# Optimization experiments

Hardware: AMD Instinct MI355X
Metric: run time of the kernel (lower is better)

The kernel has to match this reference:

```python
import jax, jax.numpy as jnp
import numpy as np

N_EMBD = 1024
N_HEAD = 16
HEAD_DIM = N_EMBD // N_HEAD


def setup_inputs() -> dict:
    key = jax.random.key(0)
    ks = jax.random.split(key, 6)
    B, T, C = 4, 2048, N_EMBD
    scale = 1.0 / np.sqrt(C)
    x = jax.random.normal(ks[0], (B, T, C), dtype=jnp.float32)
    Wq = jax.random.normal(ks[1], (C, C), dtype=jnp.float32) * scale
    Wk = jax.random.normal(ks[2], (C, C), dtype=jnp.float32) * scale
    Wv = jax.random.normal(ks[3], (C, C), dtype=jnp.float32) * scale
    Wo = jax.random.normal(ks[4], (C, C), dtype=jnp.float32) * scale
    bo = jax.random.normal(ks[5], (C,), dtype=jnp.float32) * 0.01
    return {"x": x, "Wq": Wq, "Wk": Wk, "Wv": Wv, "Wo": Wo, "bo": bo}


def reference(x, Wq, Wk, Wv, Wo, bo):
    B, T, C = x.shape
    H, D = N_HEAD, HEAD_DIM
    # projections (torch Linear: x @ W.T); reshape to [B, H, T, D]
    q = (x @ Wq.T).reshape(B, T, H, D).transpose(0, 2, 1, 3)
    k = (x @ Wk.T).reshape(B, T, H, D).transpose(0, 2, 1, 3)
    v = (x @ Wv.T).reshape(B, T, H, D).transpose(0, 2, 1, 3)
    scores = jnp.einsum("bhqd,bhkd->bhqk", q, k) / np.sqrt(D)
    causal = jnp.tril(jnp.ones((T, T), dtype=bool))  # True = keep
    scores = jnp.where(causal, scores, -jnp.inf)
    attn = jax.nn.softmax(scores, axis=-1)
    # dropout in eval mode = identity
    out = jnp.einsum("bhqk,bhkd->bhqd", attn, v)
    out = out.transpose(0, 2, 1, 3).reshape(B, T, C)
    return out @ Wo.T + bo
```

## Files before the change

### kernel.cpp

```cpp
#include <hip/hip_runtime.h>

typedef __attribute__((ext_vector_type(4))) float floatx4;
typedef __attribute__((ext_vector_type(8))) __bf16 bf16x8;
typedef __attribute__((ext_vector_type(8))) unsigned short ushort8;
typedef __attribute__((ext_vector_type(4))) unsigned short ushort4v;

#define MFMA16(a, b, c) __builtin_amdgcn_mfma_f32_16x16x32_bf16((a), (b), (c), 0, 0, 0)

static __device__ __forceinline__ unsigned short f2bu(float f) {
  unsigned int u = __builtin_bit_cast(unsigned int, f);
  unsigned int r = (u + 0x7fffu + ((u >> 16) & 1u)) >> 16;
  return (unsigned short)r;
}

static __device__ __forceinline__ unsigned int cvtpk(float lo, float hi) {
  unsigned int r;
  asm("v_cvt_pk_bf16_f32 %0, %1, %2" : "=v"(r) : "v"(lo), "v"(hi));
  return r;
}

static __device__ __forceinline__ float fexp2(float x) {
  float r;
  asm("v_exp_f32 %0, %1" : "=v"(r) : "v"(x));
  return r;
}

static __device__ __forceinline__ void gload_lds16(const void* g, void* l) {
  __builtin_amdgcn_global_load_lds((const __attribute__((address_space(1))) void*)g,
                                   (__attribute__((address_space(3))) void*)l, 16, 0, 0);
}

__global__ void cast_f32_bf16(const float* __restrict__ src, unsigned short* __restrict__ dst, int n4) {
  int i = blockIdx.x * blockDim.x + threadIdx.x;
  if (i >= n4) return;
  float4 v = reinterpret_cast<const float4*>(src)[i];
  ushort4v o;
  o.x = f2bu(v.x); o.y = f2bu(v.y); o.z = f2bu(v.z); o.w = f2bu(v.w);
  reinterpret_cast<ushort4v*>(dst)[i] = o;
}

static __device__ __forceinline__ void gemm_core(const unsigned short* __restrict__ Ag,
                                                 const unsigned short* __restrict__ Wg,
                                                 int tm0, int tn0,
                                                 unsigned short* As, unsigned short* Bs,
                                                 floatx4 acc[4][4]) {
  const int tid = threadIdx.x;
  const int w = tid >> 6, l = tid & 63;
  const int lg = l >> 4, lq = l & 15;
  const int wr = w >> 1, wc = w & 1;

  const int srow = w * 32 + (l >> 2);
  const int scol = (l & 3) * 8;
  const unsigned short* ga = Ag + (size_t)(tm0 + srow) * 1024 + scol;
  const unsigned short* gb = Wg + (size_t)(tn0 + srow) * 1024 + scol;
  unsigned short* la0 = As + (w * 32) * 32;
  unsigned short* la1 = la0 + 16 * 32;
  unsigned short* lb0 = Bs + (w * 32) * 32;
  unsigned short* lb1 = lb0 + 16 * 32;

  for (int kt = 0; kt < 32; ++kt) {
    gload_lds16(ga + kt * 32, la0);
    gload_lds16(ga + 16 * 1024 + kt * 32, la1);
    gload_lds16(gb + kt * 32, lb0);
    gload_lds16(gb + 16 * 1024 + kt * 32, lb1);
    __syncthreads();
    bf16x8 ar[4], br[4];
#pragma unroll
    for (int i = 0; i < 4; ++i) {
      ar[i] = *(const bf16x8*)(As + (wr * 64 + i * 16 + lq) * 32 + lg * 8);
      br[i] = *(const bf16x8*)(Bs + (wc * 64 + i * 16 + lq) * 32 + lg * 8);
    }
#pragma unroll
    for (int i = 0; i < 4; ++i)
#pragma unroll
      for (int j = 0; j < 4; ++j)
        acc[i][j] = MFMA16(ar[i], br[j], acc[i][j]);
    __syncthreads();
  }
}

__global__ __launch_bounds__(256) void gemm_qkv(const unsigned short* __restrict__ xb,
                                                const unsigned short* __restrict__ Wqb,
                                                const unsigned short* __restrict__ Wkb,
                                                const unsigned short* __restrict__ Wvb,
                                                unsigned short* __restrict__ Qb,
                                                unsigned short* __restrict__ Kb,
                                                unsigned short* __restrict__ Vtb) {
  __shared__ unsigned short As[128 * 32];
  __shared__ unsigned short Bs[128 * 32];
  const int tid = threadIdx.x;
  const int w = tid >> 6, l = tid & 63;
  const int lg = l >> 4, lq = l & 15;
  const int wr = w >> 1, wc = w & 1;
  const int tm0 = blockIdx.x * 128;
  const int tn0 = blockIdx.y * 128;
  const int z = blockIdx.z;
  const unsigned short* W = (z == 0) ? Wqb : (z == 1) ? Wkb : Wvb;

  floatx4 acc[4][4];
#pragma unroll
  for (int i = 0; i < 4; ++i)
#pragma unroll
    for (int j = 0; j < 4; ++j) acc[i][j] = (floatx4){0.f, 0.f, 0.f, 0.f};

  gemm_core(xb, W, tm0, tn0, As, Bs, acc);

  const int b = tm0 >> 11;
  const int t0 = tm0 & 2047;

  if (z == 2) {
#pragma unroll
    for (int mi = 0; mi < 4; ++mi)
#pragma unroll
      for (int ni = 0; ni < 4; ++ni) {
        int t = t0 + wr * 64 + mi * 16 + lg * 4;
        int n = tn0 + wc * 64 + ni * 16 + lq;
        int h = n >> 6, d = n & 63;
        ushort4v o;
        o.x = f2bu(acc[mi][ni][0]);
        o.y = f2bu(acc[mi][ni][1]);
        o.z = f2bu(acc[mi][ni][2]);
        o.w = f2bu(acc[mi][ni][3]);
        *(ushort4v*)(Vtb + ((size_t)(b * 16 + h) * 64 + d) * 2048 + t) = o;
      }
  } else {
    float sc = (z == 0) ? 0.125f * 1.44269504f : 1.0f;
    unsigned short* dst = (z == 0) ? Qb : Kb;
#pragma unroll
    for (int mi = 0; mi < 4; ++mi)
#pragma unroll
      for (int ni = 0; ni < 4; ++ni) {
        int n = tn0 + wc * 64 + ni * 16 + lq;
        int h = n >> 6, d = n & 63;
#pragma unroll
        for (int r = 0; r < 4; ++r) {
          int t = t0 + wr * 64 + mi * 16 + lg * 4 + r;
          dst[((size_t)(b * 16 + h) * 2048 + t) * 64 + d] = f2bu(acc[mi][ni][r] * sc);
        }
      }
  }
}

__global__ __launch_bounds__(256) void attn_fwd(const unsigned short* __restrict__ Qb,
                                                const unsigned short* __restrict__ Kb,
                                                const unsigned short* __restrict__ Vtb,
                                                unsigned short* __restrict__ attb) {
  constexpr int T = 2048;
  __shared__ char Ls[32768];
  const int bh = blockIdx.x;
  const int pr = blockIdx.y;
  const int tid = threadIdx.x;
  const int w = tid >> 6, l = tid & 63;
  const int lg = l >> 4, lq = l & 15;

  const char* Kgc = (const char*)(Kb + (size_t)bh * T * 64);
  const char* Vgc = (const char*)(Vtb + (size_t)bh * 64 * T);
  const unsigned short* Qp = Qb + (size_t)bh * T * 64;

  const int scolx = ((tid & 7) << 4) ^ (((tid >> 3) & 7) << 4);
  const int koff = ((tid >> 3) << 7) + scolx;
  const int voff = ((tid >> 3) << 12) + scolx;
  char* Ks = (char*)Ls;
  char* Vs = (char*)Ls + 16384;
  const int kswz = (lq & 7) << 4;
  const int wofs = w * 1024;
  const int b = bh >> 4, h = bh & 15;

  const ushort8 onesu = {0x3F80, 0x3F80, 0x3F80, 0x3F80, 0x3F80, 0x3F80, 0x3F80, 0x3F80};
  const bf16x8 onesf = __builtin_bit_cast(bf16x8, onesu);

#define STAGE(bi, kb_)                                               \
  do {                                                               \
    const char* kg_ = Kgc + (size_t)(kb_) * 128 + koff;              \
    const char* vg_ = Vgc + (size_t)(kb_) * 2 + voff;                \
    gload_lds16(kg_,          Ks + (bi) * 8192 + wofs);              \
    gload_lds16(kg_ + 4096,   Ks + (bi) * 8192 + 4096 + wofs);       \
    gload_lds16(vg_,          Vs + (bi) * 8192 + wofs);              \
    gload_lds16(vg_ + 131072, Vs + (bi) * 8192 + 4096 + wofs);       \
  } while (0)

  for (int pi = 0; pi < 2; ++pi) {
    const int qt = pi ? (31 - pr) : pr;
    const int q0 = qt * 64 + w * 16;
    const int qrow = q0 + lq;

    bf16x8 qf0 = *(const bf16x8*)(Qp + (size_t)qrow * 64 + lg * 8);
    bf16x8 qf1 = *(const bf16x8*)(Qp + (size_t)qrow * 64 + 32 + lg * 8);

    floatx4 acc[4];
#pragma unroll
    for (int dc = 0; dc < 4; ++dc) acc[dc] = (floatx4){0.f, 0.f, 0.f, 0.f};
    floatx4 rsum = (floatx4){0.f, 0.f, 0.f, 0.f};
    float m_run = -1e30f;

    int buf = 0;
    STAGE(0, 0);
    __syncthreads();

    for (int t = 0; t <= qt; ++t) {
      if (t < qt) STAGE(buf ^ 1, (t + 1) * 64);
      const char* Kl = Ks + buf * 8192;
      const char* Vl = Vs + buf * 8192;
      const int kb = t * 64;

      floatx4 s[4];
#pragma unroll
      for (int kc = 0; kc < 4; ++kc) {
        const int rowb = (kc * 16 + lq) * 128;
        bf16x8 kf0 = *(const bf16x8*)(Kl + rowb + ((lg * 16) ^ kswz));
        bf16x8 kf1 = *(const bf16x8*)(Kl + rowb + ((64 + lg * 16) ^ kswz));
        floatx4 tt = (floatx4){0.f, 0.f, 0.f, 0.f};
        tt = MFMA16(kf0, qf0, tt);
        tt = MFMA16(kf1, qf1, tt);
        s[kc] = tt;
      }

      if (t == qt) {
#pragma unroll
        for (int kc = 0; kc < 4; ++kc)
#pragma unroll
          for (int r = 0; r < 4; ++r)
            if (kb + kc * 16 + lg * 4 + r > qrow) s[kc][r] = -1e30f;
      }

      float m0 = fmaxf(fmaxf(s[0][0], s[0][1]), fmaxf(s[0][2], s[0][3]));
      float m1 = fmaxf(fmaxf(s[1][0], s[1][1]), fmaxf(s[1][2], s[1][3]));
      float m2 = fmaxf(fmaxf(s[2][0], s[2][1]), fmaxf(s[2][2], s[2][3]));
      float m3 = fmaxf(fmaxf(s[3][0], s[3][1]), fmaxf(s[3][2], s[3][3]));
      float mt = fmaxf(fmaxf(m0, m1), fmaxf(m2, m3));
      mt = fmaxf(mt, __shfl_xor(mt, 16, 64));
      mt = fmaxf(mt, __shfl_xor(mt, 32, 64));
      if (__any(mt > m_run + 11.f)) {
        float mn = fmaxf(m_run, mt);
        float corr = fexp2(m_run - mn);
#pragma unroll
        for (int dc = 0; dc < 4; ++dc) acc[dc] *= corr;
        rsum *= corr;
        m_run = mn;
      }
      float p[4][4];
#pragma unroll
      for (int kc = 0; kc < 4; ++kc)
#pragma unroll
        for (int r = 0; r < 4; ++r) p[kc][r] = fexp2(s[kc][r] - m_run);

      int4 u0, u1;
      u0.x = cvtpk(p[0][0], p[0][1]); u0.y = cvtpk(p[0][2], p[0][3]);
      u0.z = cvtpk(p[1][0], p[1][1]); u0.w = cvtpk(p[1][2], p[1][3]);
      u1.x = cvtpk(p[2][0], p[2][1]); u1.y = cvtpk(p[2][2], p[2][3]);
      u1.z = cvtpk(p[3][0], p[3][1]); u1.w = cvtpk(p[3][2], p[3][3]);
      bf16x8 pa0 = __builtin_bit_cast(bf16x8, u0);
      bf16x8 pa1 = __builtin_bit_cast(bf16x8, u1);

      rsum = MFMA16(onesf, pa0, rsum);
      rsum = MFMA16(onesf, pa1, rsum);

#pragma unroll
      for (int dc = 0; dc < 4; ++dc) {
        const int rowb = (dc * 16 + lq) * 128;
#pragma unroll
        for (int kk = 0; kk < 2; ++kk) {
          ushort4v v0 = *(const ushort4v*)(Vl + rowb + ((kk * 64 + lg * 8) ^ kswz));
          ushort4v v1 = *(const ushort4v*)(Vl + rowb + ((kk * 64 + lg * 8 + 32) ^ kswz));
          ushort8 vv = __builtin_shufflevector(v0, v1, 0, 1, 2, 3, 4, 5, 6, 7);
          bf16x8 va = __builtin_bit_cast(bf16x8, vv);
          acc[dc] = MFMA16(va, kk ? pa1 : pa0, acc[dc]);
        }
      }
      __syncthreads();
      buf ^= 1;
    }

    float inv = 1.f / rsum[0];
    unsigned short* orow = attb + (size_t)(b * 2048 + qrow) * 1024 + h * 64;
#pragma unroll
    for (int dc = 0; dc < 4; ++dc) {
      ushort4v o;
      o.x = f2bu(acc[dc][0] * inv);
      o.y = f2bu(acc[dc][1] * inv);
      o.z = f2bu(acc[dc][2] * inv);
      o.w = f2bu(acc[dc][3] * inv);
      *(ushort4v*)(orow + 16 * dc + lg * 4) = o;
    }
  }
#undef STAGE
}

__global__ __launch_bounds__(256) void gemm_out(const unsigned short* __restrict__ attb,
                                                const unsigned short* __restrict__ Wob,
                                                const float* __restrict__ bo,
                                                float* __restrict__ out) {
  __shared__ unsigned short As[128 * 32];
  __shared__ unsigned short Bs[128 * 32];
  const int tid = threadIdx.x;
  const int w = tid >> 6, l = tid & 63;
  const int lg = l >> 4, lq = l & 15;
  const int wr = w >> 1, wc = w & 1;
  const int tm0 = blockIdx.x * 128;
  const int tn0 = blockIdx.y * 128;

  floatx4 acc[4][4];
#pragma unroll
  for (int i = 0; i < 4; ++i)
#pragma unroll
    for (int j = 0; j < 4; ++j) acc[i][j] = (floatx4){0.f, 0.f, 0.f, 0.f};

  gemm_core(attb, Wob, tm0, tn0, As, Bs, acc);

#pragma unroll
  for (int mi = 0; mi < 4; ++mi)
#pragma unroll
    for (int ni = 0; ni < 4; ++ni) {
      int row = tm0 + wr * 64 + mi * 16 + lg * 4;
      int col = tn0 + wc * 64 + ni * 16 + lq;
      float bias = bo[col];
#pragma unroll
      for (int r = 0; r < 4; ++r)
        out[(size_t)(row + r) * 1024 + col] = acc[mi][ni][r] + bias;
    }
}

extern "C" void kernel_launch(void* const* d_in, const int* in_sizes, int n_in,
                              void* d_out, int out_size, void* d_ws, size_t ws_size,
                              hipStream_t stream) {
  const float* x  = (const float*)d_in[0];
  const float* Wq = (const float*)d_in[1];
  const float* Wk = (const float*)d_in[2];
  const float* Wv = (const float*)d_in[3];
  const float* Wo = (const float*)d_in[4];
  const float* bo = (const float*)d_in[5];
  float* out = (float*)d_out;

  unsigned short* ws = (unsigned short*)d_ws;
  unsigned short* xb  = ws;
  unsigned short* Wqb = ws + 8388608;
  unsigned short* Wkb = ws + 9437184;
  unsigned short* Wvb = ws + 10485760;
  unsigned short* Wob = ws + 11534336;
  unsigned short* Qb  = ws + 12582912;
  unsigned short* Kb  = ws + 20971520;
  unsigned short* Vtb = ws + 29360128;
  unsigned short* attb= ws + 37748736;

  cast_f32_bf16<<<8192, 256, 0, stream>>>(x, xb, 2097152);
  cast_f32_bf16<<<1024, 256, 0, stream>>>(Wq, Wqb, 262144);
  cast_f32_bf16<<<1024, 256, 0, stream>>>(Wk, Wkb, 262144);
  cast_f32_bf16<<<1024, 256, 0, stream>>>(Wv, Wvb, 262144);
  cast_f32_bf16<<<1024, 256, 0, stream>>>(Wo, Wob, 262144);

  gemm_qkv<<<dim3(64, 8, 3), 256, 0, stream>>>(xb, Wqb, Wkb, Wvb, Qb, Kb, Vtb);
  attn_fwd<<<dim3(64, 16), 256, 0, stream>>>(Qb, Kb, Vtb, attb);
  gemm_out<<<dim3(64, 8), 256, 0, stream>>>(attb, Wob, bo, out);
}
```

Baseline: 266.8 us.

## Double-buffer GEMM LDS tiles and merge cast kernels into one launch

The shared GEMM core now uses two LDS buffers, so the global-to-LDS load of the next K tile is issued before the MFMAs on the current tile, and one barrier per iteration is dropped. This hides load latency behind compute at the cost of twice the LDS per block, and adds a launch_bounds occupancy hint of 4 blocks. The five separate fp32-to-bf16 cast launches are merged into one kernel that picks its source buffer by index range, cutting launch overhead. There may be a race: the prefetch write into the alternate buffer relies on the previous iteration's trailing barrier, and the async global_load_lds completion depends on the barrier's implicit waitcnt.

```diff
diff --git a/kernel.cpp b/kernel.cpp
--- a/kernel.cpp
+++ b/kernel.cpp
@@ -30,13 +30,28 @@
                                    (__attribute__((address_space(3))) void*)l, 16, 0, 0);
 }
 
-__global__ void cast_f32_bf16(const float* __restrict__ src, unsigned short* __restrict__ dst, int n4) {
+__global__ void cast_all(const float* __restrict__ x,  unsigned short* __restrict__ xb,
+                         const float* __restrict__ w0, unsigned short* __restrict__ w0b,
+                         const float* __restrict__ w1, unsigned short* __restrict__ w1b,
+                         const float* __restrict__ w2, unsigned short* __restrict__ w2b,
+                         const float* __restrict__ w3, unsigned short* __restrict__ w3b) {
   int i = blockIdx.x * blockDim.x + threadIdx.x;
-  if (i >= n4) return;
-  float4 v = reinterpret_cast<const float4*>(src)[i];
+  const float* src;
+  unsigned short* dst;
+  int j;
+  if (i < 2097152) {
+    src = x; dst = xb; j = i;
+  } else {
+    j = i - 2097152;
+    int wsel = j >> 18;
+    j &= 262143;
+    src = (wsel == 0) ? w0 : (wsel == 1) ? w1 : (wsel == 2) ? w2 : w3;
+    dst = (wsel == 0) ? w0b : (wsel == 1) ? w1b : (wsel == 2) ? w2b : w3b;
+  }
+  float4 v = reinterpret_cast<const float4*>(src)[j];
   ushort4v o;
   o.x = f2bu(v.x); o.y = f2bu(v.y); o.z = f2bu(v.z); o.w = f2bu(v.w);
-  reinterpret_cast<ushort4v*>(dst)[i] = o;
+  reinterpret_cast<ushort4v*>(dst)[j] = o;
 }
 
 static __device__ __forceinline__ void gemm_core(const unsigned short* __restrict__ Ag,
@@ -53,22 +68,28 @@
   const int scol = (l & 3) * 8;
   const unsigned short* ga = Ag + (size_t)(tm0 + srow) * 1024 + scol;
   const unsigned short* gb = Wg + (size_t)(tn0 + srow) * 1024 + scol;
-  unsigned short* la0 = As + (w * 32) * 32;
-  unsigned short* la1 = la0 + 16 * 32;
-  unsigned short* lb0 = Bs + (w * 32) * 32;
-  unsigned short* lb1 = lb0 + 16 * 32;
-
+  const int ldst0 = w * 1024;
+  const int ldst1 = ldst0 + 16 * 32;
+
+#define GSTAGE(bi, kt_)                                   \
+  do {                                                    \
+    const int ko_ = (kt_) * 32;                           \
+    gload_lds16(ga + ko_,              As + (bi) * 4096 + ldst0); \
+    gload_lds16(ga + ko_ + 16 * 1024,  As + (bi) * 4096 + ldst1); \
+    gload_lds16(gb + ko_,              Bs + (bi) * 4096 + ldst0); \
+    gload_lds16(gb + ko_ + 16 * 1024,  Bs + (bi) * 4096 + ldst1); \
+  } while (0)
+
+  GSTAGE(0, 0);
+  __syncthreads();
+  int buf = 0;
   for (int kt = 0; kt < 32; ++kt) {
-    gload_lds16(ga + kt * 32, la0);
-    gload_lds16(ga + 16 * 1024 + kt * 32, la1);
-    gload_lds16(gb + kt * 32, lb0);
-    gload_lds16(gb + 16 * 1024 + kt * 32, lb1);
-    __syncthreads();
+    if (kt + 1 < 32) GSTAGE(buf ^ 1, kt + 1);
     bf16x8 ar[4], br[4];
 #pragma unroll
     for (int i = 0; i < 4; ++i) {
-      ar[i] = *(const bf16x8*)(As + (wr * 64 + i * 16 + lq) * 32 + lg * 8);
-      br[i] = *(const bf16x8*)(Bs + (wc * 64 + i * 16 + lq) * 32 + lg * 8);
+      ar[i] = *(const bf16x8*)(As + buf * 4096 + (wr * 64 + i * 16 + lq) * 32 + lg * 8);
+      br[i] = *(const bf16x8*)(Bs + buf * 4096 + (wc * 64 + i * 16 + lq) * 32 + lg * 8);
     }
 #pragma unroll
     for (int i = 0; i < 4; ++i)
@@ -76,18 +97,20 @@
       for (int j = 0; j < 4; ++j)
         acc[i][j] = MFMA16(ar[i], br[j], acc[i][j]);
     __syncthreads();
+    buf ^= 1;
   }
-}
-
-__global__ __launch_bounds__(256) void gemm_qkv(const unsigned short* __restrict__ xb,
-                                                const unsigned short* __restrict__ Wqb,
-                                                const unsigned short* __restrict__ Wkb,
-                                                const unsigned short* __restrict__ Wvb,
-                                                unsigned short* __restrict__ Qb,
-                                                unsigned short* __restrict__ Kb,
-                                                unsigned short* __restrict__ Vtb) {
-  __shared__ unsigned short As[128 * 32];
-  __shared__ unsigned short Bs[128 * 32];
+#undef GSTAGE
+}
+
+__global__ __launch_bounds__(256, 4) void gemm_qkv(const unsigned short* __restrict__ xb,
+                                                   const unsigned short* __restrict__ Wqb,
+                                                   const unsigned short* __restrict__ Wkb,
+                                                   const unsigned short* __restrict__ Wvb,
+                                                   unsigned short* __restrict__ Qb,
+                                                   unsigned short* __restrict__ Kb,
+                                                   unsigned short* __restrict__ Vtb) {
+  __shared__ unsigned short As[2 * 128 * 32];
+  __shared__ unsigned short Bs[2 * 128 * 32];
   const int tid = threadIdx.x;
   const int w = tid >> 6, l = tid & 63;
   const int lg = l >> 4, lq = l & 15;
@@ -286,12 +309,12 @@
 #undef STAGE
 }
 
-__global__ __launch_bounds__(256) void gemm_out(const unsigned short* __restrict__ attb,
-                                                const unsigned short* __restrict__ Wob,
-                                                const float* __restrict__ bo,
-                                                float* __restrict__ out) {
-  __shared__ unsigned short As[128 * 32];
-  __shared__ unsigned short Bs[128 * 32];
+__global__ __launch_bounds__(256, 4) void gemm_out(const unsigned short* __restrict__ attb,
+                                                   const unsigned short* __restrict__ Wob,
+                                                   const float* __restrict__ bo,
+                                                   float* __restrict__ out) {
+  __shared__ unsigned short As[2 * 128 * 32];
+  __shared__ unsigned short Bs[2 * 128 * 32];
   const int tid = threadIdx.x;
   const int w = tid >> 6, l = tid & 63;
   const int lg = l >> 4, lq = l & 15;
@@ -342,11 +365,7 @@
   unsigned short* Vtb = ws + 29360128;
   unsigned short* attb= ws + 37748736;
 
-  cast_f32_bf16<<<8192, 256, 0, stream>>>(x, xb, 2097152);
-  cast_f32_bf16<<<1024, 256, 0, stream>>>(Wq, Wqb, 262144);
-  cast_f32_bf16<<<1024, 256, 0, stream>>>(Wk, Wkb, 262144);
-  cast_f32_bf16<<<1024, 256, 0, stream>>>(Wv, Wvb, 262144);
-  cast_f32_bf16<<<1024, 256, 0, stream>>>(Wo, Wob, 262144);
+  cast_all<<<12288, 256, 0, stream>>>(x, xb, Wq, Wqb, Wk, Wkb, Wv, Wvb, Wo, Wob);
 
   gemm_qkv<<<dim3(64, 8, 3), 256, 0, stream>>>(xb, Wqb, Wkb, Wvb, Qb, Kb, Vtb);
   attn_fwd<<<dim3(64, 16), 256, 0, stream>>>(Qb, Kb, Vtb, attb);
```

Result: faster. 257.2 us (-3.6%).
